# Kernel optimization log

Measured on AMD Instinct MI355X. Metric: run time of the kernel, lower is better.

The kernel has to match this reference:

```python
import jax, jax.numpy as jnp
import numpy as np

EPS = 1e-5
TOP_K = 2


def setup_inputs() -> dict:
    key = jax.random.key(0)
    ks = jax.random.split(key, 8)
    B, T, D, E, F = 4, 2048, 1024, 8, 4096
    s_in = 1.0 / np.sqrt(D)
    s_ff = 1.0 / np.sqrt(F)
    return {
        "hidden_states": jax.random.normal(ks[0], (B, T, D), jnp.float32),
        "input_tensor": jax.random.normal(ks[1], (B, T, D), jnp.float32),
        "gate_w": jax.random.normal(ks[2], (D, E), jnp.float32) * s_in,
        "gate_b": jnp.zeros((E,), jnp.float32),
        "w1": jax.random.normal(ks[3], (E, D, F), jnp.float32) * s_in,
        "b1": jnp.zeros((E, F), jnp.float32),
        "w2": jax.random.normal(ks[4], (E, F, D), jnp.float32) * s_ff,
        "b2": jnp.zeros((E, D), jnp.float32),
        "gamma": jnp.ones((D,), jnp.float32),
        "beta": jnp.zeros((D,), jnp.float32),
    }


def _layer_norm(x, gamma, beta):
    mu = jnp.mean(x, axis=-1, keepdims=True)
    var = jnp.mean(jnp.square(x - mu), axis=-1, keepdims=True)
    return (x - mu) * jax.lax.rsqrt(var + EPS) * gamma + beta


def reference(hidden_states, input_tensor, gate_w, gate_b, w1, b1, w2, b2, gamma, beta):
    E = gate_b.shape[0]
    # Router: softmax over experts, then top-k gate values/indices.
    gate_logits = jnp.einsum("btd,de->bte", hidden_states, gate_w) + gate_b
    gate_probs = jax.nn.softmax(gate_logits, axis=-1)
    topk_gates, topk_idx = jax.lax.top_k(gate_probs, TOP_K)  # [B,T,K]
    # Combine weights per expert: sum of top-k gate values routed to expert e.
    combine_w = jnp.sum(
        jax.nn.one_hot(topk_idx, E, dtype=hidden_states.dtype)
        * topk_gates[..., None],
        axis=-2,
    )  # [B,T,E]
    # Dispatch/combine: weighted sum of expert FFN outputs (loop over small fixed E).
    expert_outputs = jnp.zeros_like(hidden_states)
    for e in range(E):
        h = jax.nn.gelu(jnp.einsum("btd,df->btf", hidden_states, w1[e]) + b1[e])
        y = jnp.einsum("btf,fd->btd", h, w2[e]) + b2[e]
        expert_outputs = expert_outputs + combine_w[..., e:e + 1] * y
    # Dropout is identity in eval mode.
    return _layer_norm(expert_outputs + input_tensor, gamma, beta)
```

## Files before the change

### kernel.cpp

```cpp
#include <hip/hip_runtime.h>

#define TOKENS 8192
#define DIM 1024
#define NEXP 8
#define FDIM 4096

typedef __bf16 bf16x8 __attribute__((ext_vector_type(8)));
typedef float f32x4 __attribute__((ext_vector_type(4)));

__device__ __forceinline__ unsigned short f2bf(float f) {
  unsigned u = __builtin_bit_cast(unsigned, f);
  u += 0x7fffu + ((u >> 16) & 1u);
  return (unsigned short)(u >> 16);
}

__device__ __forceinline__ float bf2f(unsigned short s) {
  unsigned u = (unsigned)s << 16;
  return __builtin_bit_cast(float, u);
}

__device__ __forceinline__ void gload16(const void* g, void* l) {
  __builtin_amdgcn_global_load_lds(
      (const __attribute__((address_space(1))) unsigned int*)g,
      (__attribute__((address_space(3))) unsigned int*)l, 16, 0, 0);
}

__global__ void zero_counts_kernel(int* counts) {
  if (threadIdx.x < NEXP) counts[threadIdx.x] = 0;
}

__global__ void scan_kernel(const int* counts, int* offs, int* nchk,
                            int* chunks0, int* chunks1) {
  if (threadIdx.x == 0) {
    int s = 0;
    for (int e = 0; e < NEXP; ++e) { offs[e] = s; s += counts[e]; }
    offs[NEXP] = s;
    int nc0 = 0, nc1 = 0;
    for (int e = 0; e < NEXP; ++e) {
      const int mt = (counts[e] + 255) >> 8;
      for (int mc = 0; mc < mt; mc += 4) {
        for (int n4 = 0; n4 < 16; n4 += 4)
          chunks0[nc0++] = (e << 16) | (mc << 8) | n4;
        chunks1[nc1++] = (e << 16) | (mc << 8);
      }
    }
    nchk[0] = nc0;
    nchk[1] = nc1;
  }
}

__global__ void router_kernel(const float* __restrict__ hs,
                              const float* __restrict__ gw,
                              const float* __restrict__ gb,
                              int* __restrict__ counts,
                              int* __restrict__ tok_idx,
                              float* __restrict__ tok_w,
                              unsigned int* __restrict__ slotinfo,
                              unsigned short* __restrict__ hs_bf) {
  const int lane = threadIdx.x & 63;
  const int wid = threadIdx.x >> 6;
  const int t = blockIdx.x * 4 + wid;
  const float* row = hs + (size_t)t * DIM;

  float x[16];
  const float4* r4 = (const float4*)(row + lane * 16);
#pragma unroll
  for (int i = 0; i < 4; ++i) {
    float4 v = r4[i];
    x[i * 4 + 0] = v.x; x[i * 4 + 1] = v.y; x[i * 4 + 2] = v.z; x[i * 4 + 3] = v.w;
  }

  float acc[8];
#pragma unroll
  for (int e = 0; e < 8; ++e) acc[e] = 0.f;
#pragma unroll
  for (int i = 0; i < 16; ++i) {
    const int d = lane * 16 + i;
    const float4* g4 = (const float4*)(gw + (size_t)d * 8);
    float4 g0 = g4[0], g1 = g4[1];
    const float xv = x[i];
    acc[0] += xv * g0.x; acc[1] += xv * g0.y; acc[2] += xv * g0.z; acc[3] += xv * g0.w;
    acc[4] += xv * g1.x; acc[5] += xv * g1.y; acc[6] += xv * g1.z; acc[7] += xv * g1.w;
  }
#pragma unroll
  for (int sh = 1; sh < 64; sh <<= 1) {
#pragma unroll
    for (int e = 0; e < 8; ++e) acc[e] += __shfl_xor(acc[e], sh, 64);
  }
#pragma unroll
  for (int e = 0; e < 8; ++e) acc[e] += gb[e];

  float mx = acc[0];
#pragma unroll
  for (int e = 1; e < 8; ++e) mx = fmaxf(mx, acc[e]);
  float p[8];
  float sum = 0.f;
#pragma unroll
  for (int e = 0; e < 8; ++e) { p[e] = __expf(acc[e] - mx); sum += p[e]; }
  const float inv = 1.0f / sum;

  int i0 = 0; float b0 = p[0];
#pragma unroll
  for (int e = 1; e < 8; ++e) if (p[e] > b0) { b0 = p[e]; i0 = e; }
  int i1 = -1; float b1v = -1.f;
#pragma unroll
  for (int e = 0; e < 8; ++e) if (e != i0 && p[e] > b1v) { b1v = p[e]; i1 = e; }

  if (lane == 0) {
    int pos0 = atomicAdd(&counts[i0], 1);
    tok_idx[i0 * TOKENS + pos0] = t;
    tok_w[i0 * TOKENS + pos0] = b0 * inv;
    int pos1 = atomicAdd(&counts[i1], 1);
    tok_idx[i1 * TOKENS + pos1] = t;
    tok_w[i1 * TOKENS + pos1] = b1v * inv;
    slotinfo[t] = ((unsigned)i0 << 29) | ((unsigned)pos0 << 16) |
                  ((unsigned)i1 << 13) | (unsigned)pos1;
  }

  unsigned short us[16];
#pragma unroll
  for (int i = 0; i < 16; ++i) us[i] = f2bf(x[i]);
  uint4 o0, o1;
  o0.x = (unsigned)us[0] | ((unsigned)us[1] << 16);
  o0.y = (unsigned)us[2] | ((unsigned)us[3] << 16);
  o0.z = (unsigned)us[4] | ((unsigned)us[5] << 16);
  o0.w = (unsigned)us[6] | ((unsigned)us[7] << 16);
  o1.x = (unsigned)us[8] | ((unsigned)us[9] << 16);
  o1.y = (unsigned)us[10] | ((unsigned)us[11] << 16);
  o1.z = (unsigned)us[12] | ((unsigned)us[13] << 16);
  o1.w = (unsigned)us[14] | ((unsigned)us[15] << 16);
  uint4* dst = (uint4*)(hs_bf + (size_t)t * DIM + lane * 16);
  dst[0] = o0;
  dst[1] = o1;
}

__global__ void cast_transpose_kernel(const float* __restrict__ src,
                                      unsigned short* __restrict__ dst,
                                      int R, int C) {
  __shared__ float tile[64][65];
  const int e = blockIdx.z;
  const int r0 = blockIdx.y * 64;
  const int c0 = blockIdx.x * 64;
  const float* s = src + (size_t)e * R * C;
  unsigned int* d = (unsigned int*)(dst + (size_t)e * R * C);

#pragma unroll
  for (int i = 0; i < 16; ++i) {
    const int idx = threadIdx.x + i * 256;
    const int r = idx >> 6;
    const int c = idx & 63;
    tile[r][c] = s[(size_t)(r0 + r) * C + (c0 + c)];
  }
  __syncthreads();
#pragma unroll
  for (int i = 0; i < 8; ++i) {
    const int idx = threadIdx.x + i * 256;
    const int c = idx >> 5;
    const int r = (idx & 31) * 2;
    unsigned pk = (unsigned)f2bf(tile[r][c]) | ((unsigned)f2bf(tile[r + 1][c]) << 16);
    d[((size_t)(c0 + c) * R + (r0 + r)) >> 1] = pk;
  }
}


#define DO_TILE(sTp, sNp, A0C, B0C, A0N, B0N, STA, STB, WSA, GATESTR, READN, FINAL)   \
  {                                                                                   \
    bf16x8 a1r[4];                                                                    \
    _Pragma("unroll") for (int f_ = 0; f_ < 4; ++f_)                                  \
      a1r[f_] = *(const bf16x8*)((sTp) + aoff[4 + f_]);                               \
    if (STA) {                                                                        \
      gload16(aS0, (WSA));                                                            \
      gload16(aS1, (WSA) + 8192);                                                     \
      aS0 += 64; aS1 += 64;                                                           \
    }                                                                                 \
    __builtin_amdgcn_sched_barrier(0);                                                \
    __builtin_amdgcn_s_setprio(1);                                                    \
    _Pragma("unroll") for (int f_ = 0; f_ < 4; ++f_)                                  \
      _Pragma("unroll") for (int g_ = 0; g_ < 4; ++g_)                                \
        acc[f_][g_] = __builtin_amdgcn_mfma_f32_16x16x32_bf16(                        \
            A0C[f_], B0C[g_], acc[f_][g_], 0, 0, 0);                                  \
    __builtin_amdgcn_s_setprio(0);                                                    \
    __builtin_amdgcn_sched_barrier(0);                                                \
    if (!(FINAL)) {                                                                   \
      asm volatile(GATESTR ::: "memory");                                             \
      __builtin_amdgcn_s_barrier();                                                   \
    }                                                                                 \
    if (READN) {                                                                      \
      _Pragma("unroll") for (int f_ = 0; f_ < 4; ++f_)                                \
        A0N[f_] = *(const bf16x8*)((sNp) + aoff[f_]);                                 \
      _Pragma("unroll") for (int g_ = 0; g_ < 4; ++g_)                                \
        B0N[g_] = *(const bf16x8*)((sNp) + 65536 + boff[g_]);                         \
    }                                                                                 \
    if (STB) {                                                                        \
      gload16(bS0, (WSA) + 65536);                                                    \
      gload16(bS1, (WSA) + 65536 + 8192);                                             \
      bS0 += 64; bS1 += 64;                                                           \
    }                                                                                 \
    __builtin_amdgcn_sched_barrier(0);                                                \
    __builtin_amdgcn_s_setprio(1);                                                    \
    _Pragma("unroll") for (int f_ = 0; f_ < 4; ++f_)                                  \
      _Pragma("unroll") for (int g_ = 0; g_ < 4; ++g_)                                \
        acc[4 + f_][g_] = __builtin_amdgcn_mfma_f32_16x16x32_bf16(                    \
            a1r[f_], B0C[g_], acc[4 + f_][g_], 0, 0, 0);                              \
    __builtin_amdgcn_s_setprio(0);                                                    \
    __builtin_amdgcn_sched_barrier(0);                                                \
  }

template<int MODE, int K, int N>
__global__ __launch_bounds__(512, 2)
void moe_gemm(const unsigned short* __restrict__ Abase,
              const unsigned short* __restrict__ Bbase,
              const float* __restrict__ bias,
              const int* __restrict__ counts,
              const int* __restrict__ offs,
              const int* __restrict__ tok_idx,
              const int* __restrict__ chunktab,
              const int* __restrict__ nchk,
              unsigned short* __restrict__ dst) {
  constexpr int NT = K / 32;
  __shared__ __align__(16) unsigned char sm[131072];

  const int L = blockIdx.x;
  const int xk = L & 7;
  const int tt = L >> 3;
  const int g = (tt >> 4) * 8 + xk;
  if (g >= nchk[MODE]) return;
  const int within = tt & 15;
  const int cd = chunktab[g];
  const int e = cd >> 16;
  const int cnt = counts[e];
  const int m0 = (((cd >> 8) & 255) + (within >> 2)) * 256;
  if (m0 >= cnt) return;
  const int n0 = ((cd & 255) + (within & 3)) * 256;
  const int goff = offs[e];

  const int tid = threadIdx.x;
  const int lane = tid & 63;
  const int wid = tid >> 6;
  const int wr = wid >> 2;
  const int wcn = wid & 3;
  const int l15 = lane & 15;
  const int cg = lane >> 4;
  const int wdst = wid * 1024;

  const int urow = tid >> 2;
  const int uchk = tid & 3;
  const int swz = uchk ^ ((urow >> 1) & 3);
  const unsigned char* Bexp = (const unsigned char*)(Bbase + (size_t)e * K * N);

  int gA0 = m0 + urow;       if (gA0 > cnt - 1) gA0 = cnt - 1;
  int gA1 = m0 + urow + 128; if (gA1 > cnt - 1) gA1 = cnt - 1;
  size_t rowA0, rowA1;
  if (MODE == 0) {
    rowA0 = (size_t)tok_idx[e * TOKENS + gA0] * K;
    rowA1 = (size_t)tok_idx[e * TOKENS + gA1] * K;
  } else {
    rowA0 = (size_t)(goff + gA0) * K;
    rowA1 = (size_t)(goff + gA1) * K;
  }
  const unsigned char* aS0 = (const unsigned char*)(Abase + rowA0) + swz * 16;
  const unsigned char* aS1 = (const unsigned char*)(Abase + rowA1) + swz * 16;
  const unsigned char* bS0 = Bexp + (size_t)(n0 + urow) * (K * 2) + swz * 16;
  const unsigned char* bS1 = Bexp + (size_t)(n0 + urow + 128) * (K * 2) + swz * 16;

  int aoff[8], boff[4];
#pragma unroll
  for (int f = 0; f < 8; ++f) {
    const int r = wr * 128 + f * 16 + l15;
    aoff[f] = r * 64 + ((cg ^ ((r >> 1) & 3)) * 16);
  }
#pragma unroll
  for (int g2 = 0; g2 < 4; ++g2) {
    const int r = wcn * 64 + g2 * 16 + l15;
    boff[g2] = r * 64 + ((cg ^ ((r >> 1) & 3)) * 16);
  }

  f32x4 acc[8][4];
  const f32x4 fz = {0.f, 0.f, 0.f, 0.f};
#pragma unroll
  for (int f = 0; f < 8; ++f)
#pragma unroll
    for (int g2 = 0; g2 < 4; ++g2) acc[f][g2] = fz;

#pragma unroll
  for (int j = 0; j < 3; ++j) {
    gload16(aS0, sm + j * 16384 + wdst);
    gload16(aS1, sm + j * 16384 + wdst + 8192);
    aS0 += 64; aS1 += 64;
    gload16(bS0, sm + 65536 + j * 16384 + wdst);
    gload16(bS1, sm + 65536 + j * 16384 + wdst + 8192);
    bS0 += 64; bS1 += 64;
  }
  asm volatile("s_waitcnt vmcnt(8)" ::: "memory");
  __builtin_amdgcn_sched_barrier(0);
  __builtin_amdgcn_s_barrier();

  const unsigned char* smc = (const unsigned char*)sm;
  bf16x8 a0A[4], b0A[4], a0B[4], b0B[4];
#pragma unroll
  for (int f = 0; f < 4; ++f) a0A[f] = *(const bf16x8*)(smc + aoff[f]);
#pragma unroll
  for (int g2 = 0; g2 < 4; ++g2) b0A[g2] = *(const bf16x8*)(smc + 65536 + boff[g2]);

  int t = 0;
#pragma unroll 1
  for (; t + 5 < NT; t += 2) {
    const unsigned char* sT0 = smc + ((t & 3) << 14);
    const unsigned char* sT1 = smc + (((t + 1) & 3) << 14);
    const unsigned char* sT2 = smc + (((t + 2) & 3) << 14);
    unsigned char* w3 = (unsigned char*)sm + (((t + 3) & 3) << 14) + wdst;
    unsigned char* w4 = (unsigned char*)sm + (((t + 4) & 3) << 14) + wdst;
    DO_TILE(sT0, sT1, a0A, b0A, a0B, b0B, 1, 1, w3,
            "s_waitcnt vmcnt(6) lgkmcnt(0)", 1, 0);
    DO_TILE(sT1, sT2, a0B, b0B, a0A, b0A, 1, 1, w4,
            "s_waitcnt vmcnt(6) lgkmcnt(0)", 1, 0);
  }
  {
    const unsigned char* sT0 = smc + ((t & 3) << 14);
    const unsigned char* sT1 = smc + (((t + 1) & 3) << 14);
    const unsigned char* sT2 = smc + (((t + 2) & 3) << 14);
    const unsigned char* sT3 = smc + (((t + 3) & 3) << 14);
    unsigned char* w3 = (unsigned char*)sm + (((t + 3) & 3) << 14) + wdst;
    DO_TILE(sT0, sT1, a0A, b0A, a0B, b0B, 1, 1, w3,
            "s_waitcnt vmcnt(6) lgkmcnt(0)", 1, 0);
    DO_TILE(sT1, sT2, a0B, b0B, a0A, b0A, 0, 0, w3,
            "s_waitcnt vmcnt(4) lgkmcnt(0)", 1, 0);
    DO_TILE(sT2, sT3, a0A, b0A, a0B, b0B, 0, 0, w3,
            "s_waitcnt vmcnt(0) lgkmcnt(0)", 1, 0);
    DO_TILE(sT3, sT3, a0B, b0B, a0A, b0A, 0, 0, w3,
            "", 0, 1);
  }

#pragma unroll
  for (int g2 = 0; g2 < 4; ++g2) {
    const int fcol = n0 + wcn * 64 + g2 * 16 + l15;
    const float bv = bias[e * N + fcol];
#pragma unroll
    for (int f = 0; f < 8; ++f) {
#pragma unroll
      for (int j = 0; j < 4; ++j) {
        const int ml = wr * 128 + f * 16 + cg * 4 + j;
        const int gm = m0 + ml;
        if (gm < cnt) {
          float v = acc[f][g2][j] + bv;
          if (MODE == 0) {
            const float u = 0.7978845608028654f * (v + 0.044715f * v * v * v);
            const float th = 1.0f - 2.0f / (1.0f + __expf(2.0f * u));
            v = 0.5f * v * (1.0f + th);
          }
          dst[(size_t)(goff + gm) * N + fcol] = f2bf(v);
        }
      }
    }
  }
}

__global__ void ln_combine_kernel(const unsigned short* __restrict__ y_buf,
                                  const float* __restrict__ in_t,
                                  const int* __restrict__ offs,
                                  const unsigned int* __restrict__ slotinfo,
                                  const float* __restrict__ tok_w,
                                  const float* __restrict__ gamma,
                                  const float* __restrict__ beta,
                                  float* __restrict__ out) {
  const int lane = threadIdx.x & 63;
  const int wid = threadIdx.x >> 6;
  const int t = blockIdx.x * 4 + wid;

  const unsigned s = slotinfo[t];
  const int e0 = s >> 29, p0 = (s >> 16) & 8191;
  const int e1 = (s >> 13) & 7, p1 = s & 8191;
  const float w0 = tok_w[e0 * TOKENS + p0];
  const float w1 = tok_w[e1 * TOKENS + p1];
  const size_t r0 = (size_t)(offs[e0] + p0) * DIM;
  const size_t r1 = (size_t)(offs[e1] + p1) * DIM;

  float v[16];
  {
    const float4* i4 = (const float4*)(in_t + (size_t)t * DIM + lane * 16);
    const uint4* y0 = (const uint4*)(y_buf + r0 + lane * 16);
    const uint4* y1 = (const uint4*)(y_buf + r1 + lane * 16);
#pragma unroll
    for (int i = 0; i < 4; ++i) {
      float4 a = i4[i];
      v[i * 4 + 0] = a.x; v[i * 4 + 1] = a.y; v[i * 4 + 2] = a.z; v[i * 4 + 3] = a.w;
    }
#pragma unroll
    for (int i = 0; i < 2; ++i) {
      uint4 u0 = y0[i];
      uint4 u1 = y1[i];
      const unsigned uw0[4] = {u0.x, u0.y, u0.z, u0.w};
      const unsigned uw1[4] = {u1.x, u1.y, u1.z, u1.w};
#pragma unroll
      for (int k = 0; k < 4; ++k) {
        const int base = i * 8 + k * 2;
        v[base + 0] += w0 * bf2f((unsigned short)(uw0[k] & 0xffff)) +
                       w1 * bf2f((unsigned short)(uw1[k] & 0xffff));
        v[base + 1] += w0 * bf2f((unsigned short)(uw0[k] >> 16)) +
                       w1 * bf2f((unsigned short)(uw1[k] >> 16));
      }
    }
  }

  float sum = 0.f, s2 = 0.f;
#pragma unroll
  for (int i = 0; i < 16; ++i) { sum += v[i]; s2 += v[i] * v[i]; }
#pragma unroll
  for (int sh = 1; sh < 64; sh <<= 1) {
    sum += __shfl_xor(sum, sh, 64);
    s2 += __shfl_xor(s2, sh, 64);
  }
  const float mu = sum * (1.0f / DIM);
  const float var = s2 * (1.0f / DIM) - mu * mu;
  const float rs = rsqrtf(var + 1e-5f);

  float4* w4 = (float4*)(out + (size_t)t * DIM + lane * 16);
#pragma unroll
  for (int i = 0; i < 4; ++i) {
    const int d = lane * 16 + i * 4;
    float4 g = *(const float4*)(gamma + d);
    float4 b = *(const float4*)(beta + d);
    float4 o;
    o.x = (v[i * 4 + 0] - mu) * rs * g.x + b.x;
    o.y = (v[i * 4 + 1] - mu) * rs * g.y + b.y;
    o.z = (v[i * 4 + 2] - mu) * rs * g.z + b.z;
    o.w = (v[i * 4 + 3] - mu) * rs * g.w + b.w;
    w4[i] = o;
  }
}

extern "C" void kernel_launch(void* const* d_in, const int* in_sizes, int n_in,
                              void* d_out, int out_size, void* d_ws, size_t ws_size,
                              hipStream_t stream) {
  const float* hs    = (const float*)d_in[0];
  const float* in_t  = (const float*)d_in[1];
  const float* gw    = (const float*)d_in[2];
  const float* gb    = (const float*)d_in[3];
  const float* w1    = (const float*)d_in[4];
  const float* b1    = (const float*)d_in[5];
  const float* w2    = (const float*)d_in[6];
  const float* b2    = (const float*)d_in[7];
  const float* gamma = (const float*)d_in[8];
  const float* beta  = (const float*)d_in[9];
  float* out = (float*)d_out;
  char* ws = (char*)d_ws;

  int* counts            = (int*)(ws + 0);
  int* offs              = (int*)(ws + 256);
  unsigned int* slotinfo = (unsigned int*)(ws + 512);
  int* nchk              = (int*)(ws + 33280);
  int* chunks0           = (int*)(ws + 33536);
  int* chunks1           = (int*)(ws + 34048);
  int* tok_idx           = (int*)(ws + 66048);
  float* tok_w           = (float*)(ws + 328192);
  unsigned short* hs_bf  = (unsigned short*)(ws + 590336);
  unsigned short* w1t    = (unsigned short*)(ws + 17367552);
  unsigned short* w2t    = (unsigned short*)(ws + 84476416);
  unsigned short* h_buf  = (unsigned short*)(ws + 151585280);
  unsigned short* y_buf  = (unsigned short*)(ws + 590336);

  zero_counts_kernel<<<1, 64, 0, stream>>>(counts);
  router_kernel<<<TOKENS / 4, 256, 0, stream>>>(hs, gw, gb, counts, tok_idx, tok_w,
                                                slotinfo, hs_bf);
  scan_kernel<<<1, 64, 0, stream>>>(counts, offs, nchk, chunks0, chunks1);
  cast_transpose_kernel<<<dim3(FDIM / 64, DIM / 64, NEXP), 256, 0, stream>>>(w1, w1t, DIM, FDIM);
  cast_transpose_kernel<<<dim3(DIM / 64, FDIM / 64, NEXP), 256, 0, stream>>>(w2, w2t, FDIM, DIM);
  moe_gemm<0, DIM, FDIM><<<1536, 512, 0, stream>>>(
      hs_bf, w1t, b1, counts, offs, tok_idx, chunks0, nchk, h_buf);
  moe_gemm<1, FDIM, DIM><<<384, 512, 0, stream>>>(
      h_buf, w2t, b2, counts, offs, tok_idx, chunks1, nchk, y_buf);
  ln_combine_kernel<<<TOKENS / 4, 256, 0, stream>>>(y_buf, in_t, offs, slotinfo,
                                                    tok_w, gamma, beta, out);
}
```

Before: 785.1 us.

## Restructure MoE GEMM pipeline to double-buffered 64-K stages and merge transpose kernels

```diff
diff --git a/kernel.cpp b/kernel.cpp
--- a/kernel.cpp
+++ b/kernel.cpp
@@ -134,15 +134,24 @@
   dst[1] = o1;
 }
 
-__global__ void cast_transpose_kernel(const float* __restrict__ src,
-                                      unsigned short* __restrict__ dst,
-                                      int R, int C) {
+__global__ void cast_transpose_all(const float* __restrict__ w1,
+                                   unsigned short* __restrict__ w1t,
+                                   const float* __restrict__ w2,
+                                   unsigned short* __restrict__ w2t) {
   __shared__ float tile[64][65];
-  const int e = blockIdx.z;
-  const int r0 = blockIdx.y * 64;
-  const int c0 = blockIdx.x * 64;
+  const int L = blockIdx.x;
+  const float* src;
+  unsigned short* dstp;
+  int R, C, bi;
+  if (L < 8192) { src = w1; dstp = w1t; R = DIM;  C = FDIM; bi = L; }
+  else          { src = w2; dstp = w2t; R = FDIM; C = DIM;  bi = L - 8192; }
+  const int nx = C >> 6;
+  const int e = bi >> 10;
+  const int w = bi & 1023;
+  const int by = w / nx, bx = w % nx;
+  const int r0 = by * 64, c0 = bx * 64;
   const float* s = src + (size_t)e * R * C;
-  unsigned int* d = (unsigned int*)(dst + (size_t)e * R * C);
+  unsigned int* d = (unsigned int*)(dstp + (size_t)e * R * C);
 
 #pragma unroll
   for (int i = 0; i < 16; ++i) {
@@ -163,47 +172,84 @@
 }
 
 
-#define DO_TILE(sTp, sNp, A0C, B0C, A0N, B0N, STA, STB, WSA, GATESTR, READN, FINAL)   \
-  {                                                                                   \
-    bf16x8 a1r[4];                                                                    \
-    _Pragma("unroll") for (int f_ = 0; f_ < 4; ++f_)                                  \
-      a1r[f_] = *(const bf16x8*)((sTp) + aoff[4 + f_]);                               \
-    if (STA) {                                                                        \
-      gload16(aS0, (WSA));                                                            \
-      gload16(aS1, (WSA) + 8192);                                                     \
-      aS0 += 64; aS1 += 64;                                                           \
-    }                                                                                 \
-    __builtin_amdgcn_sched_barrier(0);                                                \
-    __builtin_amdgcn_s_setprio(1);                                                    \
-    _Pragma("unroll") for (int f_ = 0; f_ < 4; ++f_)                                  \
-      _Pragma("unroll") for (int g_ = 0; g_ < 4; ++g_)                                \
-        acc[f_][g_] = __builtin_amdgcn_mfma_f32_16x16x32_bf16(                        \
-            A0C[f_], B0C[g_], acc[f_][g_], 0, 0, 0);                                  \
-    __builtin_amdgcn_s_setprio(0);                                                    \
-    __builtin_amdgcn_sched_barrier(0);                                                \
-    if (!(FINAL)) {                                                                   \
-      asm volatile(GATESTR ::: "memory");                                             \
-      __builtin_amdgcn_s_barrier();                                                   \
-    }                                                                                 \
-    if (READN) {                                                                      \
-      _Pragma("unroll") for (int f_ = 0; f_ < 4; ++f_)                                \
-        A0N[f_] = *(const bf16x8*)((sNp) + aoff[f_]);                                 \
-      _Pragma("unroll") for (int g_ = 0; g_ < 4; ++g_)                                \
-        B0N[g_] = *(const bf16x8*)((sNp) + 65536 + boff[g_]);                         \
-    }                                                                                 \
-    if (STB) {                                                                        \
-      gload16(bS0, (WSA) + 65536);                                                    \
-      gload16(bS1, (WSA) + 65536 + 8192);                                             \
-      bS0 += 64; bS1 += 64;                                                           \
-    }                                                                                 \
-    __builtin_amdgcn_sched_barrier(0);                                                \
-    __builtin_amdgcn_s_setprio(1);                                                    \
-    _Pragma("unroll") for (int f_ = 0; f_ < 4; ++f_)                                  \
-      _Pragma("unroll") for (int g_ = 0; g_ < 4; ++g_)                                \
-        acc[4 + f_][g_] = __builtin_amdgcn_mfma_f32_16x16x32_bf16(                    \
-            a1r[f_], B0C[g_], acc[4 + f_][g_], 0, 0, 0);                              \
-    __builtin_amdgcn_s_setprio(0);                                                    \
-    __builtin_amdgcn_sched_barrier(0);                                                \
+#define MOE_STEP(DB, NB, DOST, G1STR, DOG2)                                          \
+  {                                                                                  \
+    bf16x8 af_[4], bf_[4];                                                           \
+                                                            \
+    _Pragma("unroll") for (int f_ = 0; f_ < 4; ++f_)                                 \
+      af_[f_] = *(const bf16x8*)(smc + (DB) + aoff[f_]);                             \
+    _Pragma("unroll") for (int g_ = 0; g_ < 4; ++g_)                                 \
+      bf_[g_] = *(const bf16x8*)(smc + (DB) + 32768 + boff[g_]);                     \
+    if (DOST) { gload16(aS0, smw + (NB)); gload16(aS1, smw + (NB) + 8192); }         \
+    __builtin_amdgcn_sched_barrier(0);                                               \
+    __builtin_amdgcn_s_barrier();                                                    \
+    asm volatile("s_waitcnt lgkmcnt(0)" ::: "memory");                               \
+    __builtin_amdgcn_sched_barrier(0);                                               \
+    __builtin_amdgcn_s_setprio(1);                                                   \
+    _Pragma("unroll") for (int f_ = 0; f_ < 4; ++f_)                                 \
+      _Pragma("unroll") for (int g_ = 0; g_ < 4; ++g_)                               \
+        acc[f_][g_] = __builtin_amdgcn_mfma_f32_16x16x32_bf16(af_[f_], bf_[g_],      \
+                                                              acc[f_][g_], 0, 0, 0); \
+    __builtin_amdgcn_s_setprio(0);                                                   \
+    __builtin_amdgcn_sched_barrier(0);                                               \
+    __builtin_amdgcn_s_barrier();                                                    \
+                                                            \
+    _Pragma("unroll") for (int f_ = 0; f_ < 4; ++f_)                                 \
+      af_[f_] = *(const bf16x8*)(smc + (DB) + aoff[4 + f_]);                         \
+    if (DOST) { gload16(bS0, smw + (NB) + 32768); gload16(bS1, smw + (NB) + 40960); }\
+    __builtin_amdgcn_sched_barrier(0);                                               \
+    __builtin_amdgcn_s_barrier();                                                    \
+    asm volatile("s_waitcnt lgkmcnt(0)" ::: "memory");                               \
+    __builtin_amdgcn_sched_barrier(0);                                               \
+    __builtin_amdgcn_s_setprio(1);                                                   \
+    _Pragma("unroll") for (int f_ = 0; f_ < 4; ++f_)                                 \
+      _Pragma("unroll") for (int g_ = 0; g_ < 4; ++g_)                               \
+        acc[4 + f_][g_] = __builtin_amdgcn_mfma_f32_16x16x32_bf16(af_[f_], bf_[g_],  \
+                                                          acc[4 + f_][g_], 0, 0, 0); \
+    __builtin_amdgcn_s_setprio(0);                                                   \
+    __builtin_amdgcn_sched_barrier(0);                                               \
+    asm volatile(G1STR ::: "memory");                                                \
+    __builtin_amdgcn_s_barrier();                                                    \
+                                                            \
+    _Pragma("unroll") for (int f_ = 0; f_ < 4; ++f_)                                 \
+      af_[f_] = *(const bf16x8*)(smc + (DB) + 16384 + aoff[f_]);                     \
+    _Pragma("unroll") for (int g_ = 0; g_ < 4; ++g_)                                 \
+      bf_[g_] = *(const bf16x8*)(smc + (DB) + 49152 + boff[g_]);                     \
+    if (DOST) { gload16(aS0 + 64, smw + (NB) + 16384);                               \
+                gload16(aS1 + 64, smw + (NB) + 24576); }                             \
+    __builtin_amdgcn_sched_barrier(0);                                               \
+    __builtin_amdgcn_s_barrier();                                                    \
+    asm volatile("s_waitcnt lgkmcnt(0)" ::: "memory");                               \
+    __builtin_amdgcn_sched_barrier(0);                                               \
+    __builtin_amdgcn_s_setprio(1);                                                   \
+    _Pragma("unroll") for (int f_ = 0; f_ < 4; ++f_)                                 \
+      _Pragma("unroll") for (int g_ = 0; g_ < 4; ++g_)                               \
+        acc[f_][g_] = __builtin_amdgcn_mfma_f32_16x16x32_bf16(af_[f_], bf_[g_],      \
+                                                              acc[f_][g_], 0, 0, 0); \
+    __builtin_amdgcn_s_setprio(0);                                                   \
+    __builtin_amdgcn_sched_barrier(0);                                               \
+    __builtin_amdgcn_s_barrier();                                                    \
+                                                            \
+    _Pragma("unroll") for (int f_ = 0; f_ < 4; ++f_)                                 \
+      af_[f_] = *(const bf16x8*)(smc + (DB) + 16384 + aoff[4 + f_]);                 \
+    if (DOST) { gload16(bS0 + 64, smw + (NB) + 49152);                               \
+                gload16(bS1 + 64, smw + (NB) + 57344);                               \
+                aS0 += 128; aS1 += 128; bS0 += 128; bS1 += 128; }                    \
+    __builtin_amdgcn_sched_barrier(0);                                               \
+    __builtin_amdgcn_s_barrier();                                                    \
+    asm volatile("s_waitcnt lgkmcnt(0)" ::: "memory");                               \
+    __builtin_amdgcn_sched_barrier(0);                                               \
+    __builtin_amdgcn_s_setprio(1);                                                   \
+    _Pragma("unroll") for (int f_ = 0; f_ < 4; ++f_)                                 \
+      _Pragma("unroll") for (int g_ = 0; g_ < 4; ++g_)                               \
+        acc[4 + f_][g_] = __builtin_amdgcn_mfma_f32_16x16x32_bf16(af_[f_], bf_[g_],  \
+                                                          acc[4 + f_][g_], 0, 0, 0); \
+    __builtin_amdgcn_s_setprio(0);                                                   \
+    __builtin_amdgcn_sched_barrier(0);                                               \
+    if (DOG2) {                                                                      \
+      asm volatile("s_waitcnt vmcnt(4)" ::: "memory");                               \
+      __builtin_amdgcn_s_barrier();                                                  \
+    }                                                                                \
   }
 
 template<int MODE, int K, int N>
@@ -217,7 +263,7 @@
               const int* __restrict__ chunktab,
               const int* __restrict__ nchk,
               unsigned short* __restrict__ dst) {
-  constexpr int NT = K / 32;
+  constexpr int NS = K / 64;
   __shared__ __align__(16) unsigned char sm[131072];
 
   const int L = blockIdx.x;
@@ -282,54 +328,25 @@
 #pragma unroll
     for (int g2 = 0; g2 < 4; ++g2) acc[f][g2] = fz;
 
-#pragma unroll
-  for (int j = 0; j < 3; ++j) {
-    gload16(aS0, sm + j * 16384 + wdst);
-    gload16(aS1, sm + j * 16384 + wdst + 8192);
-    aS0 += 64; aS1 += 64;
-    gload16(bS0, sm + 65536 + j * 16384 + wdst);
-    gload16(bS1, sm + 65536 + j * 16384 + wdst + 8192);
-    bS0 += 64; bS1 += 64;
-  }
-  asm volatile("s_waitcnt vmcnt(8)" ::: "memory");
+  const unsigned char* smc = (const unsigned char*)sm;
+  unsigned char* smw = (unsigned char*)sm + wdst;
+
+  gload16(aS0, smw);                gload16(aS1, smw + 8192);
+  gload16(bS0, smw + 32768);        gload16(bS1, smw + 40960);
+  gload16(aS0 + 64, smw + 16384);   gload16(aS1 + 64, smw + 24576);
+  gload16(bS0 + 64, smw + 49152);   gload16(bS1 + 64, smw + 57344);
+  aS0 += 128; aS1 += 128; bS0 += 128; bS1 += 128;
+  asm volatile("s_waitcnt vmcnt(4)" ::: "memory");
   __builtin_amdgcn_sched_barrier(0);
   __builtin_amdgcn_s_barrier();
 
-  const unsigned char* smc = (const unsigned char*)sm;
-  bf16x8 a0A[4], b0A[4], a0B[4], b0B[4];
-#pragma unroll
-  for (int f = 0; f < 4; ++f) a0A[f] = *(const bf16x8*)(smc + aoff[f]);
-#pragma unroll
-  for (int g2 = 0; g2 < 4; ++g2) b0A[g2] = *(const bf16x8*)(smc + 65536 + boff[g2]);
-
-  int t = 0;
 #pragma unroll 1
-  for (; t + 5 < NT; t += 2) {
-    const unsigned char* sT0 = smc + ((t & 3) << 14);
-    const unsigned char* sT1 = smc + (((t + 1) & 3) << 14);
-    const unsigned char* sT2 = smc + (((t + 2) & 3) << 14);
-    unsigned char* w3 = (unsigned char*)sm + (((t + 3) & 3) << 14) + wdst;
-    unsigned char* w4 = (unsigned char*)sm + (((t + 4) & 3) << 14) + wdst;
-    DO_TILE(sT0, sT1, a0A, b0A, a0B, b0B, 1, 1, w3,
-            "s_waitcnt vmcnt(6) lgkmcnt(0)", 1, 0);
-    DO_TILE(sT1, sT2, a0B, b0B, a0A, b0A, 1, 1, w4,
-            "s_waitcnt vmcnt(6) lgkmcnt(0)", 1, 0);
-  }
-  {
-    const unsigned char* sT0 = smc + ((t & 3) << 14);
-    const unsigned char* sT1 = smc + (((t + 1) & 3) << 14);
-    const unsigned char* sT2 = smc + (((t + 2) & 3) << 14);
-    const unsigned char* sT3 = smc + (((t + 3) & 3) << 14);
-    unsigned char* w3 = (unsigned char*)sm + (((t + 3) & 3) << 14) + wdst;
-    DO_TILE(sT0, sT1, a0A, b0A, a0B, b0B, 1, 1, w3,
-            "s_waitcnt vmcnt(6) lgkmcnt(0)", 1, 0);
-    DO_TILE(sT1, sT2, a0B, b0B, a0A, b0A, 0, 0, w3,
-            "s_waitcnt vmcnt(4) lgkmcnt(0)", 1, 0);
-    DO_TILE(sT2, sT3, a0A, b0A, a0B, b0B, 0, 0, w3,
-            "s_waitcnt vmcnt(0) lgkmcnt(0)", 1, 0);
-    DO_TILE(sT3, sT3, a0B, b0B, a0A, b0A, 0, 0, w3,
-            "", 0, 1);
-  }
+  for (int it = 0; it < (NS - 2) / 2; ++it) {
+    MOE_STEP(0,     65536, 1, "s_waitcnt vmcnt(4)", 1);
+    MOE_STEP(65536, 0,     1, "s_waitcnt vmcnt(4)", 1);
+  }
+  MOE_STEP(0,     65536, 1, "s_waitcnt vmcnt(4)", 1);
+  MOE_STEP(65536, 0,     0, "s_waitcnt vmcnt(0)", 0);
 
 #pragma unroll
   for (int g2 = 0; g2 < 4; ++g2) {
@@ -418,13 +435,13 @@
 #pragma unroll
   for (int i = 0; i < 4; ++i) {
     const int d = lane * 16 + i * 4;
-    float4 g = *(const float4*)(gamma + d);
-    float4 b = *(const float4*)(beta + d);
+    float4 gg = *(const float4*)(gamma + d);
+    float4 bb = *(const float4*)(beta + d);
     float4 o;
-    o.x = (v[i * 4 + 0] - mu) * rs * g.x + b.x;
-    o.y = (v[i * 4 + 1] - mu) * rs * g.y + b.y;
-    o.z = (v[i * 4 + 2] - mu) * rs * g.z + b.z;
-    o.w = (v[i * 4 + 3] - mu) * rs * g.w + b.w;
+    o.x = (v[i * 4 + 0] - mu) * rs * gg.x + bb.x;
+    o.y = (v[i * 4 + 1] - mu) * rs * gg.y + bb.y;
+    o.z = (v[i * 4 + 2] - mu) * rs * gg.z + bb.z;
+    o.w = (v[i * 4 + 3] - mu) * rs * gg.w + bb.w;
     w4[i] = o;
   }
 }
@@ -463,8 +480,7 @@
   router_kernel<<<TOKENS / 4, 256, 0, stream>>>(hs, gw, gb, counts, tok_idx, tok_w,
                                                 slotinfo, hs_bf);
   scan_kernel<<<1, 64, 0, stream>>>(counts, offs, nchk, chunks0, chunks1);
-  cast_transpose_kernel<<<dim3(FDIM / 64, DIM / 64, NEXP), 256, 0, stream>>>(w1, w1t, DIM, FDIM);
-  cast_transpose_kernel<<<dim3(DIM / 64, FDIM / 64, NEXP), 256, 0, stream>>>(w2, w2t, FDIM, DIM);
+  cast_transpose_all<<<16384, 256, 0, stream>>>(w1, w1t, w2, w2t);
   moe_gemm<0, DIM, FDIM><<<1536, 512, 0, stream>>>(
       hs_bf, w1t, b1, counts, offs, tok_idx, chunks0, nchk, h_buf);
   moe_gemm<1, FDIM, DIM><<<384, 512, 0, stream>>>(
```

Result: no change. 796.8 us (+1.5%).
